# Kernel optimization log

Hardware: AMD Instinct MI355X
Metric: run time of the kernel (lower is better)

## Reference

```python
import jax, jax.numpy as jnp
import numpy as np

HIDDEN = 64
NUM_LAYERS = 6
BN_EPS = 1e-5


def setup_inputs() -> dict:
    key = jax.random.key(0)
    N, M = 1024, 1024
    num_nodes = N + M
    ks = jax.random.split(key, 12)
    x = jax.random.normal(ks[0], (num_nodes, 2), dtype=jnp.float32)
    # complete bipartite edges: (a, N+b) for all a in [0,N), b in [0,M), row-major so view(N,M) is meaningful
    row = jnp.repeat(jnp.arange(N, dtype=jnp.int64), M)
    col = N + jnp.tile(jnp.arange(M, dtype=jnp.int64), N)
    edge_index = jnp.stack([row, col], axis=0)
    s = 1.0 / np.sqrt(HIDDEN)
    return {
        "x": x,
        "edge_index": edge_index,
        "in_w": jax.random.normal(ks[1], (2, HIDDEN), jnp.float32) * 0.5,
        "in_b": jnp.zeros((HIDDEN,), jnp.float32),
        "conv_w": jax.random.normal(ks[2], (NUM_LAYERS, HIDDEN, HIDDEN), jnp.float32) * s,
        "conv_b": jnp.zeros((NUM_LAYERS, HIDDEN), jnp.float32),
        "bn_gamma": jnp.ones((NUM_LAYERS, HIDDEN), jnp.float32),
        "bn_beta": jnp.zeros((NUM_LAYERS, HIDDEN), jnp.float32),
        "out_w": jax.random.normal(ks[3], (2 * HIDDEN, 1), jnp.float32) * s,
        "out_b": jnp.zeros((1,), jnp.float32),
        "N": N,
        "M": M,
    }


def reference(x, edge_index, in_w, in_b, conv_w, conv_b, bn_gamma, bn_beta, out_w, out_b, N, M):
    num_nodes = x.shape[0]
    # GCN normalization with added self-loops (PyG GCNConv defaults)
    loops = jnp.arange(num_nodes, dtype=edge_index.dtype)
    row = jnp.concatenate([edge_index[0], loops])
    col = jnp.concatenate([edge_index[1], loops])
    deg = jax.ops.segment_sum(jnp.ones_like(col, dtype=x.dtype), col, num_segments=num_nodes)
    dinv = jnp.where(deg > 0, jax.lax.rsqrt(deg), 0.0)
    norm = dinv[row] * dinv[col]  # [E+num_nodes]

    h = jax.nn.relu(x @ in_w + in_b)
    for i in range(NUM_LAYERS):
        h_res = h
        hw = h @ conv_w[i]
        agg = jax.ops.segment_sum(hw[row] * norm[:, None], col, num_segments=num_nodes)
        h = agg + conv_b[i]
        # BatchNorm1d in training mode: batch stats, biased variance
        mu = h.mean(axis=0)
        var = ((h - mu) ** 2).mean(axis=0)
        h = (h - mu) * jax.lax.rsqrt(var + BN_EPS) * bn_gamma[i] + bn_beta[i]
        h = jax.nn.relu(h)
        if i > 0 and i % 2 == 1:
            h = h + h_res

    ef = jnp.concatenate([h[edge_index[0]], h[edge_index[1]]], axis=1)  # [E, 2H]
    scores = (ef @ out_w + out_b)[:, 0]
    return scores.reshape(N, M)
```

## Files before the change

### kernel.cpp

```cpp
#include <hip/hip_runtime.h>


#define NBLK 64
#define MAGIC 0x13572468u

__device__ __forceinline__ float relu_(float x) { return x > 0.f ? x : 0.f; }

#define AT_LOAD(p)    __hip_atomic_load((p), __ATOMIC_RELAXED, __HIP_MEMORY_SCOPE_AGENT)
#define AT_STORE(p,v) __hip_atomic_store((p), (v), __ATOMIC_RELAXED, __HIP_MEMORY_SCOPE_AGENT)
#define AT_ADD(p,v)   __hip_atomic_fetch_add((p), (v), __ATOMIC_RELAXED, __HIP_MEMORY_SCOPE_AGENT)

#define PART_OFF  768
#define UV_OFF    13056
#define FLAG_OFF  15104

__global__ __launch_bounds__(256, 1) void k_fused(
    const float* __restrict__ x,
    const float* __restrict__ in_w, const float* __restrict__ in_b,
    const float* __restrict__ conv_w,
    const float* __restrict__ bn_g, const float* __restrict__ bn_b,
    const float* __restrict__ out_w,
    unsigned int* __restrict__ ws)
{
    __shared__ float Wl[2][4096];
    __shared__ float hl[2048];
    __shared__ float Pp[3 * 2048];
    __shared__ float pcoef[64], scoef[64];
    __shared__ float g_lds[384], b_lds[384];
    __shared__ float ow_lds[128];

    const int t = threadIdx.x, b = blockIdx.x;
    const int w    = t >> 6;
    const int lane = t & 63;
    const int fi   = lane & 7;
    const int f0   = fi * 8;
    const int ng   = lane >> 3;
    const int n0   = ng * 4;
    const int sw   = ng & 3;
    const int kb   = w * 16;
    const bool isA = b < 32;
    float* part = (float*)(ws + PART_OFF);
    float* uv   = (float*)(ws + UV_OFF);

    {
        const float4* src = (const float4*)conv_w;
        float4* dst = (float4*)Wl[0];
        dst[t]       = src[t];
        dst[t + 256] = src[t + 256];
        dst[t + 512] = src[t + 512];
        dst[t + 768] = src[t + 768];
        for (int i = t; i < 384; i += 256) { g_lds[i] = bn_g[i]; b_lds[i] = bn_b[i]; }
        if (t < 128) ow_lds[t] = out_w[t];
    }

    if (b == 0) {
        for (int i = t; i < PART_OFF + 12288; i += 256) AT_STORE(ws + i, 0u);
        asm volatile("s_waitcnt vmcnt(0)" ::: "memory");
        __syncthreads();
        if (t == 0) AT_STORE(ws + FLAG_OFF, MAGIC);
    }

    {
        const int nl = t >> 3, fj = (t & 7) * 8;
        const int rsw = (nl >> 2) & 3;
        const int node = b * 32 + nl;
        float x0 = x[node * 2], x1 = x[node * 2 + 1];
#pragma unroll
        for (int j = 0; j < 8; j++) {
            int f = fj + j;
            float v = relu_(fmaf(x0, in_w[f], fmaf(x1, in_w[64 + f], in_b[f])));
            hl[nl * 64 + ((((f >> 2)) ^ rsw) << 2) + (f & 3)] = v;
        }
    }
    __syncthreads();

    for (int layer = 0; layer < 6; layer++) {
        const float* Wb = Wl[layer & 1];
        float acc[4][8];
#pragma unroll
        for (int n = 0; n < 4; n++)
#pragma unroll
            for (int j = 0; j < 8; j++) acc[n][j] = 0.f;

#pragma unroll
        for (int kk = 0; kk < 16; kk += 4) {
            const int cb = (kb + kk) >> 2;
            float hv[4][4];
#pragma unroll
            for (int n = 0; n < 4; n++) {
                float4 h4 = *(const float4*)&hl[(n0 + n) * 64 + ((cb ^ sw) << 2)];
                hv[n][0] = h4.x; hv[n][1] = h4.y; hv[n][2] = h4.z; hv[n][3] = h4.w;
            }
#pragma unroll
            for (int j = 0; j < 4; j++) {
                const float* wr = Wb + (kb + kk + j) * 64 + f0;
                float4 w0 = *(const float4*)wr;
                float4 w1 = *(const float4*)(wr + 4);
                float wv[8] = {w0.x, w0.y, w0.z, w0.w, w1.x, w1.y, w1.z, w1.w};
#pragma unroll
                for (int n = 0; n < 4; n++)
#pragma unroll
                    for (int q = 0; q < 8; q++)
                        acc[n][q] = fmaf(hv[n][j], wv[q], acc[n][q]);
            }
        }

        float4 pf[6];
        const int idx = (w - 1) * 64 + lane;
        if (w > 0) {
            if (layer < 5) {
                const float4* src = (const float4*)(conv_w + (layer + 1) * 4096);
#pragma unroll
                for (int r = 0; r < 5; r++) pf[r] = src[idx + 192 * r];
                if (idx < 64) pf[5] = src[idx + 960];
            }
            float* Pw = Pp + (w - 1) * 2048;
#pragma unroll
            for (int n = 0; n < 4; n++) {
                float* prow = Pw + (n0 + n) * 64;
                *(float4*)&prow[((2 * fi)     ^ sw) << 2] =
                    make_float4(acc[n][0], acc[n][1], acc[n][2], acc[n][3]);
                *(float4*)&prow[((2 * fi + 1) ^ sw) << 2] =
                    make_float4(acc[n][4], acc[n][5], acc[n][6], acc[n][7]);
            }
        }
        __syncthreads();

        if (w > 0) {
            if (layer < 5) {
                float4* dst = (float4*)Wl[(layer + 1) & 1];
#pragma unroll
                for (int r = 0; r < 5; r++) dst[idx + 192 * r] = pf[r];
                if (idx < 64) dst[idx + 960] = pf[5];
            }
        } else {
#pragma unroll
            for (int r = 0; r < 3; r++) {
                const float* Pr = Pp + r * 2048;
#pragma unroll
                for (int n = 0; n < 4; n++) {
                    const float* prow = Pr + (n0 + n) * 64;
                    float4 p0 = *(const float4*)&prow[((2 * fi)     ^ sw) << 2];
                    float4 p1 = *(const float4*)&prow[((2 * fi + 1) ^ sw) << 2];
                    acc[n][0] += p0.x; acc[n][1] += p0.y; acc[n][2] += p0.z; acc[n][3] += p0.w;
                    acc[n][4] += p1.x; acc[n][5] += p1.y; acc[n][6] += p1.z; acc[n][7] += p1.w;
                }
            }
            float sv[8], qv[8];
#pragma unroll
            for (int j = 0; j < 8; j++) {
                sv[j] = (acc[0][j] + acc[1][j]) + (acc[2][j] + acc[3][j]);
                qv[j] = fmaf(acc[0][j], acc[0][j], fmaf(acc[1][j], acc[1][j],
                        fmaf(acc[2][j], acc[2][j], acc[3][j] * acc[3][j])));
            }
#pragma unroll
            for (int m = 8; m < 64; m <<= 1) {
#pragma unroll
                for (int j = 0; j < 8; j++) {
                    sv[j] += __shfl_xor(sv[j], m);
                    qv[j] += __shfl_xor(qv[j], m);
                }
            }
            if (layer == 0) { while (AT_LOAD(ws + FLAG_OFF) != MAGIC) {} }

            {
                float* base = part + layer * 2048 + (b & 7) * 256 + (isA ? 0 : 128);
                AT_ADD(base + f0 + ng, sv[ng]);
                AT_ADD(base + 64 + f0 + ng, qv[ng]);
            }
            asm volatile("s_waitcnt vmcnt(0)" ::: "memory");
            if (lane == 0) AT_ADD(ws + layer * 128 + (b & 3) * 32, 1u);

            float SA, QA, SB, QB;
            {
                const float* p = part + layer * 2048 + lane;
                const unsigned int* c = ws + layer * 128;
                for (;;) {
                    unsigned c0 = AT_LOAD(c);
                    unsigned c1 = AT_LOAD(c + 32);
                    unsigned c2 = AT_LOAD(c + 64);
                    unsigned c3 = AT_LOAD(c + 96);
                    float a0 = 0.f, a1 = 0.f, a2 = 0.f, a3 = 0.f;
#pragma unroll
                    for (int r = 0; r < 8; r++) {
                        a0 += AT_LOAD(p + r * 256);
                        a1 += AT_LOAD(p + r * 256 + 64);
                        a2 += AT_LOAD(p + r * 256 + 128);
                        a3 += AT_LOAD(p + r * 256 + 192);
                    }
                    if (c0 + c1 + c2 + c3 == NBLK) { SA = a0; QA = a1; SB = a2; QB = a3; break; }
                }
            }

            {
                const float c1 = 9.75609756097561e-4f;
                const float c2 = 3.1234752377721214e-2f;
                float sumAgg = SA + c1 * SB + 1024.f * c2 * SA;
                float sumSq  = QA + c1 * c1 * QB + 2.f * c1 * c2 * SA * SB
                             + 1024.f * c2 * c2 * SA * SA;
                float meanAgg = sumAgg * (1.f / 2048.f);
                float var = sumSq * (1.f / 2048.f) - meanAgg * meanAgg;
                float rstd = rsqrtf(var + 1e-5f);
                float scale = rstd * g_lds[layer * 64 + lane];
                float bt = b_lds[layer * 64 + lane];
                if (isA) { pcoef[lane] = scale;      scoef[lane] = bt - meanAgg * scale; }
                else     { pcoef[lane] = c1 * scale; scoef[lane] = bt + (c2 * SA - meanAgg) * scale; }
            }
            float pc[8], sc[8];
            {
                float4 p0 = *(const float4*)&pcoef[f0];
                float4 p1 = *(const float4*)&pcoef[f0 + 4];
                float4 s0 = *(const float4*)&scoef[f0];
                float4 s1 = *(const float4*)&scoef[f0 + 4];
                pc[0] = p0.x; pc[1] = p0.y; pc[2] = p0.z; pc[3] = p0.w;
                pc[4] = p1.x; pc[5] = p1.y; pc[6] = p1.z; pc[7] = p1.w;
                sc[0] = s0.x; sc[1] = s0.y; sc[2] = s0.z; sc[3] = s0.w;
                sc[4] = s1.x; sc[5] = s1.y; sc[6] = s1.z; sc[7] = s1.w;
            }

            float vals[4][8];
#pragma unroll
            for (int n = 0; n < 4; n++)
#pragma unroll
                for (int j = 0; j < 8; j++)
                    vals[n][j] = relu_(fmaf(acc[n][j], pc[j], sc[j]));
            if (layer == 1 || layer == 3 || layer == 5) {
#pragma unroll
                for (int n = 0; n < 4; n++) {
                    const float* hrow = hl + (n0 + n) * 64;
                    float4 r0 = *(const float4*)&hrow[((2 * fi)     ^ sw) << 2];
                    float4 r1 = *(const float4*)&hrow[((2 * fi + 1) ^ sw) << 2];
                    vals[n][0] += r0.x; vals[n][1] += r0.y; vals[n][2] += r0.z; vals[n][3] += r0.w;
                    vals[n][4] += r1.x; vals[n][5] += r1.y; vals[n][6] += r1.z; vals[n][7] += r1.w;
                }
            }
            if (layer < 5) {
#pragma unroll
                for (int n = 0; n < 4; n++) {
                    float* hrow = hl + (n0 + n) * 64;
                    *(float4*)&hrow[((2 * fi)     ^ sw) << 2] =
                        make_float4(vals[n][0], vals[n][1], vals[n][2], vals[n][3]);
                    *(float4*)&hrow[((2 * fi + 1) ^ sw) << 2] =
                        make_float4(vals[n][4], vals[n][5], vals[n][6], vals[n][7]);
                }
            } else {
                const float* wv = ow_lds + (isA ? 0 : 64) + f0;
                float4 o0 = *(const float4*)wv;
                float4 o1 = *(const float4*)(wv + 4);
                float d[4];
#pragma unroll
                for (int n = 0; n < 4; n++) {
                    d[n] = fmaf(vals[n][0], o0.x, fmaf(vals[n][1], o0.y,
                           fmaf(vals[n][2], o0.z, fmaf(vals[n][3], o0.w,
                           fmaf(vals[n][4], o1.x, fmaf(vals[n][5], o1.y,
                           fmaf(vals[n][6], o1.z, vals[n][7] * o1.w)))))));
                    d[n] += __shfl_xor(d[n], 1);
                    d[n] += __shfl_xor(d[n], 2);
                    d[n] += __shfl_xor(d[n], 4);
                }
                if (fi == 0) {
#pragma unroll
                    for (int n = 0; n < 4; n++)
                        AT_STORE(uv + b * 32 + n0 + n, d[n]);
                }
            }
        }
        __syncthreads();
    }
}

__global__ __launch_bounds__(256) void k_out(const float* __restrict__ uv,
                                             const float* __restrict__ out_b,
                                             float* __restrict__ out) {
    const int a = blockIdx.x;
    const int t = threadIdx.x;
    float ua = uv[a] + out_b[0];
    float4 vv = ((const float4*)(uv + 1024))[t];
    ((float4*)(out + a * 1024))[t] =
        make_float4(ua + vv.x, ua + vv.y, ua + vv.z, ua + vv.w);
}

extern "C" void kernel_launch(void* const* d_in, const int* in_sizes, int n_in,
                              void* d_out, int out_size, void* d_ws, size_t ws_size,
                              hipStream_t stream) {
    const float* x      = (const float*)d_in[0];
    const float* in_w   = (const float*)d_in[2];
    const float* in_b   = (const float*)d_in[3];
    const float* conv_w = (const float*)d_in[4];
    const float* bn_g   = (const float*)d_in[6];
    const float* bn_b   = (const float*)d_in[7];
    const float* out_w  = (const float*)d_in[8];
    const float* out_b  = (const float*)d_in[9];
    float* out = (float*)d_out;

    unsigned int* ws = (unsigned int*)d_ws;
    const float* uv = (const float*)(ws + UV_OFF);

    k_fused<<<NBLK, 256, 0, stream>>>(x, in_w, in_b, conv_w, bn_g, bn_b,
                                      out_w, ws);
    k_out<<<1024, 256, 0, stream>>>(uv, out_b, out);
}
```

Before: 109.9 us.

## Replace atomic BN stat accumulation with per-block slot stores and lane-0 barrier

Each block now writes its per-feature sum and sum-of-squares partials with plain atomic stores into its own slot of a per-layer array, instead of float atomic adds into shared partial buckets. This also removes the need to zero the partial region at startup. Only lane 0 of each wave spins on the grid-barrier counter, with s_sleep backoff, and the wave then reduces all 64 block slots using vectorised float4 loads. The goal is to cut atomic contention and the repeated polling of partial sums during the cross-block barrier. The risk is visibility: the slot reads after the barrier are ordinary loads ordered only by a compiler fence and relaxed atomics, so they could in principle read stale data.

```diff
diff --git a/kernel.cpp b/kernel.cpp
--- a/kernel.cpp
+++ b/kernel.cpp
@@ -10,9 +10,9 @@
 #define AT_STORE(p,v) __hip_atomic_store((p), (v), __ATOMIC_RELAXED, __HIP_MEMORY_SCOPE_AGENT)
 #define AT_ADD(p,v)   __hip_atomic_fetch_add((p), (v), __ATOMIC_RELAXED, __HIP_MEMORY_SCOPE_AGENT)
 
-#define PART_OFF  768
-#define UV_OFF    13056
-#define FLAG_OFF  15104
+#define ST_OFF    768
+#define UV_OFF    49920
+#define FLAG_OFF  51968
 
 __global__ __launch_bounds__(256, 1) void k_fused(
     const float* __restrict__ x,
@@ -39,8 +39,8 @@
     const int sw   = ng & 3;
     const int kb   = w * 16;
     const bool isA = b < 32;
-    float* part = (float*)(ws + PART_OFF);
-    float* uv   = (float*)(ws + UV_OFF);
+    float* stf = (float*)(ws + ST_OFF);
+    float* uv  = (float*)(ws + UV_OFF);
 
     {
         const float4* src = (const float4*)conv_w;
@@ -54,7 +54,7 @@
     }
 
     if (b == 0) {
-        for (int i = t; i < PART_OFF + 12288; i += 256) AT_STORE(ws + i, 0u);
+        for (int i = t; i < 768; i += 256) AT_STORE(ws + i, 0u);
         asm volatile("s_waitcnt vmcnt(0)" ::: "memory");
         __syncthreads();
         if (t == 0) AT_STORE(ws + FLAG_OFF, MAGIC);
@@ -161,35 +161,43 @@
                     qv[j] += __shfl_xor(qv[j], m);
                 }
             }
-            if (layer == 0) { while (AT_LOAD(ws + FLAG_OFF) != MAGIC) {} }
 
             {
-                float* base = part + layer * 2048 + (b & 7) * 256 + (isA ? 0 : 128);
-                AT_ADD(base + f0 + ng, sv[ng]);
-                AT_ADD(base + 64 + f0 + ng, qv[ng]);
+                float* sp = stf + layer * 8192 + (f0 + ng) * 128 + b;
+                AT_STORE(sp, sv[ng]);
+                AT_STORE(sp + 64, qv[ng]);
             }
             asm volatile("s_waitcnt vmcnt(0)" ::: "memory");
-            if (lane == 0) AT_ADD(ws + layer * 128 + (b & 3) * 32, 1u);
-
-            float SA, QA, SB, QB;
-            {
-                const float* p = part + layer * 2048 + lane;
+
+            if (lane == 0) {
+                if (layer == 0) {
+                    while (AT_LOAD(ws + FLAG_OFF) != MAGIC)
+                        __builtin_amdgcn_s_sleep(1);
+                }
+                AT_ADD(ws + layer * 128 + (b & 3) * 32, 1u);
                 const unsigned int* c = ws + layer * 128;
                 for (;;) {
                     unsigned c0 = AT_LOAD(c);
                     unsigned c1 = AT_LOAD(c + 32);
                     unsigned c2 = AT_LOAD(c + 64);
                     unsigned c3 = AT_LOAD(c + 96);
-                    float a0 = 0.f, a1 = 0.f, a2 = 0.f, a3 = 0.f;
-#pragma unroll
-                    for (int r = 0; r < 8; r++) {
-                        a0 += AT_LOAD(p + r * 256);
-                        a1 += AT_LOAD(p + r * 256 + 64);
-                        a2 += AT_LOAD(p + r * 256 + 128);
-                        a3 += AT_LOAD(p + r * 256 + 192);
-                    }
-                    if (c0 + c1 + c2 + c3 == NBLK) { SA = a0; QA = a1; SB = a2; QB = a3; break; }
-                }
+                    if (c0 + c1 + c2 + c3 == NBLK) break;
+                    __builtin_amdgcn_s_sleep(2);
+                }
+            }
+            asm volatile("" ::: "memory");
+
+            float SA = 0.f, QA = 0.f, SB = 0.f, QB = 0.f;
+            {
+                const float4* sp = (const float4*)(stf + layer * 8192 + lane * 128);
+#pragma unroll
+                for (int i = 0; i < 8; i++)  { float4 v = sp[i];      SA += (v.x + v.y) + (v.z + v.w); }
+#pragma unroll
+                for (int i = 8; i < 16; i++) { float4 v = sp[i];      SB += (v.x + v.y) + (v.z + v.w); }
+#pragma unroll
+                for (int i = 16; i < 24; i++){ float4 v = sp[i];      QA += (v.x + v.y) + (v.z + v.w); }
+#pragma unroll
+                for (int i = 24; i < 32; i++){ float4 v = sp[i];      QB += (v.x + v.y) + (v.z + v.w); }
             }
 
             {
```

Result: slower. 117.8 us (+7.2%).
